# Performance work log

Measured on AMD Instinct MI355X. Metric: run time of the kernel, lower is better.

The kernel has to match this reference:

```python
import jax, jax.numpy as jnp
import numpy as np

EMBED = 1024
HEADS = 16
HEAD_DIM = EMBED // HEADS


def setup_inputs() -> dict:
    key = jax.random.key(0)
    ks = jax.random.split(key, 8)
    N, S = 4, 2048
    values = jax.random.normal(ks[0], (N, S, EMBED), dtype=jnp.float32)
    queries = jax.random.normal(ks[1], (N, S, EMBED), dtype=jnp.float32)
    keys = jax.random.normal(ks[2], (N, S, EMBED), dtype=jnp.float32)
    mask = jax.random.randint(ks[3], (N, 1, S, S), 0, 2, dtype=jnp.int32)
    sc = 1.0 / np.sqrt(HEAD_DIM)
    Wv = jax.random.normal(ks[4], (HEAD_DIM, HEAD_DIM), dtype=jnp.float32) * sc
    Wk = jax.random.normal(ks[5], (HEAD_DIM, HEAD_DIM), dtype=jnp.float32) * sc
    Wq = jax.random.normal(ks[6], (HEAD_DIM, HEAD_DIM), dtype=jnp.float32) * sc
    Wo = jax.random.normal(ks[7], (EMBED, EMBED), dtype=jnp.float32) * (1.0 / np.sqrt(EMBED))
    bo = jnp.zeros((EMBED,), dtype=jnp.float32)
    return {"values": values, "queries": queries, "keys": keys, "mask": mask,
            "Wv": Wv, "Wk": Wk, "Wq": Wq, "Wo": Wo, "bo": bo}


def reference(values, queries, keys, mask, Wv, Wk, Wq, Wo, bo):
    N, S, _ = queries.shape
    # split heads: (N, len, H, D)
    v = values.reshape(N, -1, HEADS, HEAD_DIM)
    k = keys.reshape(N, -1, HEADS, HEAD_DIM)
    q = queries.reshape(N, -1, HEADS, HEAD_DIM)
    # per-head linear projections (nn.Linear: y = x @ W.T, no bias)
    v = jnp.einsum('nlhd,ed->nlhe', v, Wv)
    k = jnp.einsum('nlhd,ed->nlhe', k, Wk)
    q = jnp.einsum('nlhd,ed->nlhe', q, Wq)
    # energy: (N, H, q_len, k_len)
    energy = jnp.einsum('nqhd,nkhd->nhqk', q, k)
    energy = jnp.where(mask == 0, jnp.float32(-1e20), energy)
    # non-standard scale: sqrt(embed_size), applied after masking
    attn = jax.nn.softmax(energy / jnp.sqrt(jnp.float32(EMBED)), axis=3)
    out = jnp.einsum('nhql,nlhd->nqhd', attn, v).reshape(N, S, EMBED)
    return out @ Wo.T + bo
```

## Files before the change

### kernel.cpp

```cpp
#include <hip/hip_runtime.h>
#include <hip/hip_bf16.h>

#define NBATCH 4
#define SEQ    2048
#define EMBED  1024
#define HEADS  16
#define HD     64

typedef __attribute__((ext_vector_type(8))) short bf16x8;
typedef __attribute__((ext_vector_type(4))) float f32x4;

__device__ __forceinline__ short f2bf(float f) {
  union { float f; unsigned u; } v; v.f = f;
  unsigned r = v.u + 0x7fffu + ((v.u >> 16) & 1u);
  return (short)(r >> 16);
}

__device__ __forceinline__ unsigned pkbf(float a, float b) {
#if __has_builtin(__builtin_amdgcn_cvt_pk_bf16_f32)
  typedef __attribute__((ext_vector_type(2))) __bf16 bf16x2_t;
  bf16x2_t r = __builtin_amdgcn_cvt_pk_bf16_f32(a, b);
  union { bf16x2_t v; unsigned u; } cv; cv.v = r; return cv.u;
#else
  return (unsigned)(unsigned short)f2bf(a) | ((unsigned)(unsigned short)f2bf(b) << 16);
#endif
}

typedef __attribute__((address_space(1))) const void gas_void;
typedef __attribute__((address_space(3))) void las_void;
__device__ __forceinline__ void glds16(const void* g, void* l) {
  __builtin_amdgcn_global_load_lds((gas_void*)g, (las_void*)l, 16, 0, 0);
}

#define C2 0.04508422f

__global__ __launch_bounds__(256) void cvt_all(
    const float* __restrict__ Wo, const float* __restrict__ Wq,
    const float* __restrict__ Wk, const float* __restrict__ Wv,
    short* __restrict__ dWo, short* __restrict__ dWq,
    short* __restrict__ dWk, short* __restrict__ dWv)
{
  int e = (blockIdx.x * 256 + threadIdx.x) * 4;
  const float* src; short* dst; int off; float sc = 1.0f;
  if (e < EMBED * EMBED) { src = Wo; dst = dWo; off = e; }
  else {
    int j = e - EMBED * EMBED;
    if      (j < 4096)  { src = Wq; dst = dWq; off = j; sc = C2; }
    else if (j < 8192)  { src = Wk; dst = dWk; off = j - 4096; }
    else if (j < 12288) { src = Wv; dst = dWv; off = j - 8192; }
    else return;
  }
  float4 v = *(const float4*)(src + off);
  ushort4 p;
  p.x = (unsigned short)f2bf(v.x * sc);
  p.y = (unsigned short)f2bf(v.y * sc);
  p.z = (unsigned short)f2bf(v.z * sc);
  p.w = (unsigned short)f2bf(v.w * sc);
  *(ushort4*)(dst + off) = p;
}

__global__ __launch_bounds__(256) void mask_pack(const int* __restrict__ mask,
                                                 unsigned long long* __restrict__ bits) {
  long long t = (long long)blockIdx.x * 256 + threadIdx.x;
  int lane = threadIdx.x & 63;
  int m = mask[t];
  unsigned long long b = __ballot(m != 0);
  if (lane == 0) bits[t >> 6] = b;
}

__global__ __launch_bounds__(256) void proj_kernel(
    const float* __restrict__ srcQ, const float* __restrict__ srcK, const float* __restrict__ srcV,
    const short* __restrict__ WbQ, const short* __restrict__ WbK, const short* __restrict__ WbV,
    short* __restrict__ Qp, short* __restrict__ Kp, short* __restrict__ Vt)
{
  int rt = blockIdx.x;
  int h  = blockIdx.y;
  int mz = blockIdx.z;
  const float* src = (mz == 0) ? srcQ : ((mz == 1) ? srcK : srcV);
  const short* Wb  = (mz == 0) ? WbQ : ((mz == 1) ? WbK : WbV);

  __shared__ __align__(16) short At[64][72];

  int tid = threadIdx.x;
  int r0 = rt * 64;
  for (int idx = tid; idx < 64 * 16; idx += 256) {
    int row = idx >> 4;
    int c4  = idx & 15;
    float4 v = *(const float4*)(src + (long long)(r0 + row) * EMBED + h * HD + c4 * 4);
    uint2 pk2;
    pk2.x = pkbf(v.x, v.y);
    pk2.y = pkbf(v.z, v.w);
    *(uint2*)&At[row][c4 * 4] = pk2;
  }
  __syncthreads();

  int lane = tid & 63, w = tid >> 6, quad = lane >> 4, l15 = lane & 15;

  bf16x8 af0 = *(const bf16x8*)&At[w * 16 + l15][quad * 8];
  bf16x8 af1 = *(const bf16x8*)&At[w * 16 + l15][32 + quad * 8];

  f32x4 acc[4];
  for (int cg = 0; cg < 4; cg++) {
    acc[cg] = (f32x4){0.f, 0.f, 0.f, 0.f};
    bf16x8 b0 = *(const bf16x8*)(Wb + (cg * 16 + l15) * 64 + quad * 8);
    bf16x8 b1 = *(const bf16x8*)(Wb + (cg * 16 + l15) * 64 + 32 + quad * 8);
    acc[cg] = __builtin_amdgcn_mfma_f32_16x16x32_bf16(af0, b0, acc[cg], 0, 0, 0);
    acc[cg] = __builtin_amdgcn_mfma_f32_16x16x32_bf16(af1, b1, acc[cg], 0, 0, 0);
  }

  int rloc = w * 16 + quad * 4;
  if (mz < 2) {
    short* dst = (mz == 0) ? Qp : Kp;
    for (int cg = 0; cg < 4; cg++) {
      for (int reg = 0; reg < 4; reg++) {
        int r = r0 + rloc + reg;
        int n = r >> 11, s = r & 2047;
        dst[((long long)(n * HEADS + h) * SEQ + s) * HD + cg * 16 + l15] = f2bf(acc[cg][reg]);
      }
    }
  } else {
    int r = r0 + rloc;
    int n = r >> 11, s = r & 2047;
    for (int cg = 0; cg < 4; cg++) {
      int d = cg * 16 + l15;
      uint2 pk2;
      pk2.x = pkbf(acc[cg][0], acc[cg][1]);
      pk2.y = pkbf(acc[cg][2], acc[cg][3]);
      *(uint2*)(Vt + ((long long)(n * HEADS + h) * HD + d) * SEQ + s) = pk2;
    }
  }
}

__global__ __launch_bounds__(512) void attn_kernel(
    const short* __restrict__ Qp, const short* __restrict__ Kp, const short* __restrict__ Vt,
    const unsigned long long* __restrict__ mbits, short* __restrict__ AO)
{
  int qt = blockIdx.x, h = blockIdx.y, nb = blockIdx.z;
  int q0 = qt * 128;

  __shared__ __align__(16) short KtL[2][64 * 64];
  __shared__ __align__(16) short VsL[2][64 * 64];
  __shared__ __align__(16) short Pls[8][16][72];

  int tid = threadIdx.x, lane = tid & 63, w = tid >> 6, quad = lane >> 4, l15 = lane & 15;
  int g8 = lane & 7, r8 = lane >> 3;
  int swz = g8 ^ r8;
  int s3 = l15 & 7;
  int o0 = (quad ^ s3) * 16;
  int o1 = ((quad + 4) ^ s3) * 16;

  long long nh = (long long)(nb * HEADS + h);
  const char* Kb = (const char*)(Kp + nh * SEQ * HD);
  const char* Vb = (const char*)(Vt + nh * HD * SEQ);
  const short* Qbase = Qp + (nh * SEQ + q0) * HD;

  int qrow = q0 + w * 16 + l15;

  int kgo = (w * 8 + r8) * 128 + swz * 16;
  int vgo = (w * 8 + r8) * 4096 + swz * 16;
  unsigned klo = (unsigned)(w * 8) * 128;

  const unsigned long long* mptr = mbits + ((long long)nb * SEQ + qrow) * 32;

  bf16x8 qf0 = *(const bf16x8*)(Qbase + (w * 16 + l15) * HD + quad * 8);
  bf16x8 qf1 = *(const bf16x8*)(Qbase + (w * 16 + l15) * HD + 32 + quad * 8);

  f32x4 O[4];
#pragma unroll
  for (int i = 0; i < 4; i++) O[i] = (f32x4){0.f, 0.f, 0.f, 0.f};
  float lsum = 0.f;

  glds16(Kb + kgo, (char*)KtL[0] + klo);
  glds16(Vb + vgo, (char*)VsL[0] + klo);
  unsigned long long mrow_nxt = mptr[0];

  for (int kt = 0; kt < 32; kt++) {
    __syncthreads();

    if (kt < 31) {
      int k1 = (kt + 1) * 64;
      glds16(Kb + k1 * 128 + kgo, (char*)KtL[(kt + 1) & 1] + klo);
      glds16(Vb + k1 * 2   + vgo, (char*)VsL[(kt + 1) & 1] + klo);
    }
    unsigned long long mrow = mrow_nxt;
    if (kt < 31) mrow_nxt = mptr[kt + 1];

    const char* KB = (const char*)KtL[kt & 1];
    f32x4 sA[4];
#pragma unroll
    for (int cg = 0; cg < 4; cg++) {
      bf16x8 kf0 = *(const bf16x8*)(KB + (cg * 16 + l15) * 128 + o0);
      bf16x8 kf1 = *(const bf16x8*)(KB + (cg * 16 + l15) * 128 + o1);
      f32x4 a = (f32x4){0.f, 0.f, 0.f, 0.f};
      a = __builtin_amdgcn_mfma_f32_16x16x32_bf16(kf0, qf0, a, 0, 0, 0);
      a = __builtin_amdgcn_mfma_f32_16x16x32_bf16(kf1, qf1, a, 0, 0, 0);
      sA[cg] = a;
    }

    unsigned mlo = (unsigned)mrow, mhi = (unsigned)(mrow >> 32);
    unsigned sh = (unsigned)(quad * 4);
    unsigned nibs[4];
    nibs[0] = (mlo >> sh) & 0xFu;
    nibs[1] = (mlo >> (sh + 16)) & 0xFu;
    nibs[2] = (mhi >> sh) & 0xFu;
    nibs[3] = (mhi >> (sh + 16)) & 0xFu;

#pragma unroll
    for (int cg = 0; cg < 4; cg++) {
#pragma unroll
      for (int r = 0; r < 4; r++) {
        float p = __builtin_amdgcn_exp2f(sA[cg][r]);
        p = (nibs[cg] & (1u << r)) ? p : 0.f;
        sA[cg][r] = p;
      }
    }
    {
      float a0 = (sA[0][0] + sA[0][1]) + (sA[0][2] + sA[0][3]);
      float a1 = (sA[1][0] + sA[1][1]) + (sA[1][2] + sA[1][3]);
      float a2 = (sA[2][0] + sA[2][1]) + (sA[2][2] + sA[2][3]);
      float a3 = (sA[3][0] + sA[3][1]) + (sA[3][2] + sA[3][3]);
      lsum += (a0 + a1) + (a2 + a3);
    }

#pragma unroll
    for (int cg = 0; cg < 4; cg++) {
      uint2 pk;
      pk.x = pkbf(sA[cg][0], sA[cg][1]);
      pk.y = pkbf(sA[cg][2], sA[cg][3]);
      *(uint2*)&Pls[w][l15][cg * 16 + quad * 4] = pk;
    }

    bf16x8 pa0 = *(const bf16x8*)&Pls[w][l15][quad * 8];
    bf16x8 pa1 = *(const bf16x8*)&Pls[w][l15][32 + quad * 8];

    const char* VB = (const char*)VsL[kt & 1];
#pragma unroll
    for (int cg = 0; cg < 4; cg++) {
      bf16x8 vf0 = *(const bf16x8*)(VB + (cg * 16 + l15) * 128 + o0);
      bf16x8 vf1 = *(const bf16x8*)(VB + (cg * 16 + l15) * 128 + o1);
      O[cg] = __builtin_amdgcn_mfma_f32_16x16x32_bf16(vf0, pa0, O[cg], 0, 0, 0);
      O[cg] = __builtin_amdgcn_mfma_f32_16x16x32_bf16(vf1, pa1, O[cg], 0, 0, 0);
    }
  }

  lsum += __shfl_xor(lsum, 16);
  lsum += __shfl_xor(lsum, 32);
  float inv = 1.f / lsum;
  short* aoRow = AO + ((long long)nb * SEQ + qrow) * EMBED + h * HD;
#pragma unroll
  for (int cg = 0; cg < 4; cg++) {
    uint2 pk;
    pk.x = pkbf(O[cg][0] * inv, O[cg][1] * inv);
    pk.y = pkbf(O[cg][2] * inv, O[cg][3] * inv);
    *(uint2*)(aoRow + cg * 16 + quad * 4) = pk;
  }
}

__global__ __launch_bounds__(256) void outproj_kernel(
    const short* __restrict__ AO, const short* __restrict__ Wob,
    const float* __restrict__ bo, float* __restrict__ out)
{
  int rt = blockIdx.x, ct = blockIdx.y;
  __shared__ __align__(16) short AtL[128 * 64];
  __shared__ __align__(16) short BtL[128 * 64];

  int tid = threadIdx.x, lane = tid & 63, w = tid >> 6, quad = lane >> 4, l15 = lane & 15;
  int g8 = lane & 7, r8 = lane >> 3;
  int swz = g8 ^ r8;
  int s3 = l15 & 7;
  int o0 = (quad ^ s3) * 16;
  int o1 = ((quad + 4) ^ s3) * 16;

  int r0 = rt * 128, c0 = ct * 128;
  int wr = (w >> 1) * 64, wc = (w & 1) * 64;

  const char* Abase = (const char*)AO  + (long long)(r0 + w * 8 + r8) * 2048 + swz * 16;
  const char* Bbase = (const char*)Wob + (long long)(c0 + w * 8 + r8) * 2048 + swz * 16;
  unsigned lbase = (unsigned)(w * 8) * 128;

  f32x4 acc[4][4];
#pragma unroll
  for (int mi = 0; mi < 4; mi++)
#pragma unroll
    for (int ni = 0; ni < 4; ni++) acc[mi][ni] = (f32x4){0.f, 0.f, 0.f, 0.f};

  for (int kc = 0; kc < 16; kc++) {
    __syncthreads();
#pragma unroll
    for (int i = 0; i < 4; i++) {
      glds16(Abase + (long long)i * 32 * 2048 + kc * 128, (char*)AtL + lbase + i * 32 * 128);
      glds16(Bbase + (long long)i * 32 * 2048 + kc * 128, (char*)BtL + lbase + i * 32 * 128);
    }
    __syncthreads();

    const char* AB = (const char*)AtL;
    const char* BB = (const char*)BtL;
    bf16x8 af[4][2], bf[4][2];
#pragma unroll
    for (int mi = 0; mi < 4; mi++) {
      int r = wr + mi * 16 + l15;
      af[mi][0] = *(const bf16x8*)(AB + r * 128 + o0);
      af[mi][1] = *(const bf16x8*)(AB + r * 128 + o1);
    }
#pragma unroll
    for (int ni = 0; ni < 4; ni++) {
      int r = wc + ni * 16 + l15;
      bf[ni][0] = *(const bf16x8*)(BB + r * 128 + o0);
      bf[ni][1] = *(const bf16x8*)(BB + r * 128 + o1);
    }
#pragma unroll
    for (int mi = 0; mi < 4; mi++)
#pragma unroll
      for (int ni = 0; ni < 4; ni++) {
        acc[mi][ni] = __builtin_amdgcn_mfma_f32_16x16x32_bf16(af[mi][0], bf[ni][0], acc[mi][ni], 0, 0, 0);
        acc[mi][ni] = __builtin_amdgcn_mfma_f32_16x16x32_bf16(af[mi][1], bf[ni][1], acc[mi][ni], 0, 0, 0);
      }
  }

#pragma unroll
  for (int ni = 0; ni < 4; ni++) {
    float b = bo[c0 + wc + ni * 16 + l15];
#pragma unroll
    for (int mi = 0; mi < 4; mi++)
#pragma unroll
      for (int reg = 0; reg < 4; reg++) {
        int r = r0 + wr + mi * 16 + quad * 4 + reg;
        out[(long long)r * EMBED + c0 + wc + ni * 16 + l15] = acc[mi][ni][reg] + b;
      }
  }
}

extern "C" void kernel_launch(void* const* d_in, const int* in_sizes, int n_in,
                              void* d_out, int out_size, void* d_ws, size_t ws_size,
                              hipStream_t stream) {
  const float* values  = (const float*)d_in[0];
  const float* queries = (const float*)d_in[1];
  const float* keys    = (const float*)d_in[2];
  const int*   mask    = (const int*)d_in[3];
  const float* Wv = (const float*)d_in[4];
  const float* Wk = (const float*)d_in[5];
  const float* Wq = (const float*)d_in[6];
  const float* Wo = (const float*)d_in[7];
  const float* bo = (const float*)d_in[8];
  float* out = (float*)d_out;

  char* ws = (char*)d_ws;
  size_t off = 0;
  const size_t PROJ_BYTES = (size_t)NBATCH * HEADS * SEQ * HD * 2;
  short* Qp = (short*)(ws + off); off += PROJ_BYTES;
  short* Kp = (short*)(ws + off); off += PROJ_BYTES;
  short* Vt = (short*)(ws + off); off += PROJ_BYTES;
  short* AO = (short*)(ws + off); off += PROJ_BYTES;
  unsigned long long* mbits = (unsigned long long*)(ws + off);
  off += (size_t)NBATCH * SEQ * (SEQ / 64) * 8;
  short* Wob = (short*)(ws + off); off += (size_t)EMBED * EMBED * 2;
  short* WbQ = (short*)(ws + off); off += HD * HD * 2;
  short* WbK = (short*)(ws + off); off += HD * HD * 2;
  short* WbV = (short*)(ws + off); off += HD * HD * 2;

  cvt_all<<<dim3((EMBED * EMBED + 3 * HD * HD) / 4 / 256), dim3(256), 0, stream>>>(
      Wo, Wq, Wk, Wv, Wob, WbQ, WbK, WbV);

  mask_pack<<<dim3((NBATCH * SEQ * SEQ) / 256), dim3(256), 0, stream>>>(mask, mbits);

  proj_kernel<<<dim3((NBATCH * SEQ) / 64, HEADS, 3), dim3(256), 0, stream>>>(
      queries, keys, values, WbQ, WbK, WbV, Qp, Kp, Vt);

  attn_kernel<<<dim3(SEQ / 128, HEADS, NBATCH), dim3(512), 0, stream>>>(Qp, Kp, Vt, mbits, AO);

  outproj_kernel<<<dim3((NBATCH * SEQ) / 128, EMBED / 128), dim3(256), 0, stream>>>(AO, Wob, bo, out);
}
```

Baseline: 377.1 us.

## Rewrite attention with 32x32 MFMA, in-register P via permlane32 swap

The attention kernel now uses 32x32x16 bf16 MFMA tiles with 4 waves each owning 32 query rows, instead of 16x16x32 tiles with 8 waves. The softmax probabilities are repacked in registers with v_permlane32_swap into the B-operand layout, removing the per-wave LDS round trip for P. The loop is manually unrolled by two so buffer indices are compile-time constants. This aims to cut LDS traffic and instruction overhead and raise MFMA efficiency, at the cost of more registers per thread and fewer threads per block.

```diff
diff --git a/kernel.cpp b/kernel.cpp
--- a/kernel.cpp
+++ b/kernel.cpp
@@ -9,6 +9,7 @@
 
 typedef __attribute__((ext_vector_type(8))) short bf16x8;
 typedef __attribute__((ext_vector_type(4))) float f32x4;
+typedef __attribute__((ext_vector_type(16))) float f32x16;
 
 __device__ __forceinline__ short f2bf(float f) {
   union { float f; unsigned u; } v; v.f = f;
@@ -31,6 +32,17 @@
 __device__ __forceinline__ void glds16(const void* g, void* l) {
   __builtin_amdgcn_global_load_lds((gas_void*)g, (las_void*)l, 16, 0, 0);
 }
+
+__device__ __forceinline__ bf16x8 mk8(unsigned a, unsigned b, unsigned c, unsigned d) {
+  union { unsigned u[4]; bf16x8 v; } t;
+  t.u[0] = a; t.u[1] = b; t.u[2] = c; t.u[3] = d; return t.v;
+}
+
+__device__ __forceinline__ void pl32swap(unsigned &a, unsigned &b) {
+  asm volatile("v_permlane32_swap_b32 %0, %1" : "+v"(a), "+v"(b));
+}
+
+#define MFMA32(A, B, C) __builtin_amdgcn_mfma_f32_32x32x16_bf16((A), (B), (C), 0, 0, 0)
 
 #define C2 0.04508422f
 
@@ -131,128 +143,148 @@
   }
 }
 
-__global__ __launch_bounds__(512) void attn_kernel(
+#define SOFTMAX_KK(SV, MW, PAV0, PAV1) do {                                       \
+    unsigned n0 = ((MW) >> sh4) & 0xFu;                                           \
+    unsigned n1 = ((MW) >> (sh4 + 8)) & 0xFu;                                     \
+    unsigned n2 = ((MW) >> (sh4 + 16)) & 0xFu;                                    \
+    unsigned n3 = ((MW) >> (sh4 + 24)) & 0xFu;                                    \
+    float p0  = __builtin_amdgcn_exp2f(SV[0]);   p0  = (n0 & 1u) ? p0  : 0.f;     \
+    float p1  = __builtin_amdgcn_exp2f(SV[1]);   p1  = (n0 & 2u) ? p1  : 0.f;     \
+    float p2  = __builtin_amdgcn_exp2f(SV[2]);   p2  = (n0 & 4u) ? p2  : 0.f;     \
+    float p3  = __builtin_amdgcn_exp2f(SV[3]);   p3  = (n0 & 8u) ? p3  : 0.f;     \
+    float p4  = __builtin_amdgcn_exp2f(SV[4]);   p4  = (n1 & 1u) ? p4  : 0.f;     \
+    float p5  = __builtin_amdgcn_exp2f(SV[5]);   p5  = (n1 & 2u) ? p5  : 0.f;     \
+    float p6  = __builtin_amdgcn_exp2f(SV[6]);   p6  = (n1 & 4u) ? p6  : 0.f;     \
+    float p7  = __builtin_amdgcn_exp2f(SV[7]);   p7  = (n1 & 8u) ? p7  : 0.f;     \
+    float p8  = __builtin_amdgcn_exp2f(SV[8]);   p8  = (n2 & 1u) ? p8  : 0.f;     \
+    float p9  = __builtin_amdgcn_exp2f(SV[9]);   p9  = (n2 & 2u) ? p9  : 0.f;     \
+    float p10 = __builtin_amdgcn_exp2f(SV[10]);  p10 = (n2 & 4u) ? p10 : 0.f;     \
+    float p11 = __builtin_amdgcn_exp2f(SV[11]);  p11 = (n2 & 8u) ? p11 : 0.f;     \
+    float p12 = __builtin_amdgcn_exp2f(SV[12]);  p12 = (n3 & 1u) ? p12 : 0.f;     \
+    float p13 = __builtin_amdgcn_exp2f(SV[13]);  p13 = (n3 & 2u) ? p13 : 0.f;     \
+    float p14 = __builtin_amdgcn_exp2f(SV[14]);  p14 = (n3 & 4u) ? p14 : 0.f;     \
+    float p15 = __builtin_amdgcn_exp2f(SV[15]);  p15 = (n3 & 8u) ? p15 : 0.f;     \
+    lsum += (((p0 + p1) + (p2 + p3)) + ((p4 + p5) + (p6 + p7)))                   \
+          + (((p8 + p9) + (p10 + p11)) + ((p12 + p13) + (p14 + p15)));            \
+    unsigned u0 = pkbf(p0, p1),   u1 = pkbf(p2, p3);                              \
+    unsigned u2 = pkbf(p4, p5),   u3 = pkbf(p6, p7);                              \
+    unsigned u4 = pkbf(p8, p9),   u5 = pkbf(p10, p11);                            \
+    unsigned u6 = pkbf(p12, p13), u7 = pkbf(p14, p15);                            \
+    pl32swap(u0, u2); pl32swap(u1, u3);                                           \
+    pl32swap(u4, u6); pl32swap(u5, u7);                                           \
+    PAV0 = mk8(u0, u1, u2, u3);                                                   \
+    PAV1 = mk8(u4, u5, u6, u7);                                                   \
+  } while (0)
+
+#define ATTN_ITER(BUF, KT) do {                                                   \
+    __syncthreads();                                                              \
+    if ((KT) < 31) {                                                              \
+      const char* ks_ = Kb + ((KT) + 1) * 8192 + kgo;                             \
+      const char* vs_ = Vb + ((KT) + 1) * 128 + vgo;                              \
+      char* kd_ = ldsK + (((BUF) ^ 1) * 8192) + klo;                              \
+      char* vd_ = ldsV + (((BUF) ^ 1) * 8192) + klo;                              \
+      glds16(ks_,          kd_);                                                  \
+      glds16(ks_ + 4096,   kd_ + 4096);                                           \
+      glds16(vs_,          vd_);                                                  \
+      glds16(vs_ + 131072, vd_ + 4096);                                           \
+      mnxt = mptr[(KT) + 1];                                                      \
+    }                                                                             \
+    unsigned mlo = (unsigned)mcur, mhiw = (unsigned)(mcur >> 32);                 \
+    const char* KB_ = ldsK + (BUF) * 8192;                                        \
+    const char* VB_ = ldsV + (BUF) * 8192;                                        \
+    bf16x8 pa0, pa1, pa2, pa3;                                                    \
+    {                                                                             \
+      f32x16 s = {};                                                              \
+      s = MFMA32(*(const bf16x8*)(KB_ + a4_0), qf0, s);                           \
+      s = MFMA32(*(const bf16x8*)(KB_ + a4_1), qf1, s);                           \
+      s = MFMA32(*(const bf16x8*)(KB_ + a4_2), qf2, s);                           \
+      s = MFMA32(*(const bf16x8*)(KB_ + a4_3), qf3, s);                           \
+      SOFTMAX_KK(s, mlo, pa0, pa1);                                               \
+    }                                                                             \
+    {                                                                             \
+      f32x16 s = {};                                                              \
+      s = MFMA32(*(const bf16x8*)(KB_ + 4096 + a4_0), qf0, s);                    \
+      s = MFMA32(*(const bf16x8*)(KB_ + 4096 + a4_1), qf1, s);                    \
+      s = MFMA32(*(const bf16x8*)(KB_ + 4096 + a4_2), qf2, s);                    \
+      s = MFMA32(*(const bf16x8*)(KB_ + 4096 + a4_3), qf3, s);                    \
+      SOFTMAX_KK(s, mhiw, pa2, pa3);                                              \
+    }                                                                             \
+    O0 = MFMA32(*(const bf16x8*)(VB_ + a4_0),        pa0, O0);                    \
+    O1 = MFMA32(*(const bf16x8*)(VB_ + 4096 + a4_0), pa0, O1);                    \
+    O0 = MFMA32(*(const bf16x8*)(VB_ + a4_1),        pa1, O0);                    \
+    O1 = MFMA32(*(const bf16x8*)(VB_ + 4096 + a4_1), pa1, O1);                    \
+    O0 = MFMA32(*(const bf16x8*)(VB_ + a4_2),        pa2, O0);                    \
+    O1 = MFMA32(*(const bf16x8*)(VB_ + 4096 + a4_2), pa2, O1);                    \
+    O0 = MFMA32(*(const bf16x8*)(VB_ + a4_3),        pa3, O0);                    \
+    O1 = MFMA32(*(const bf16x8*)(VB_ + 4096 + a4_3), pa3, O1);                    \
+    mcur = mnxt;                                                                  \
+  } while (0)
+
+__global__ __launch_bounds__(256, 4) void attn_kernel(
     const short* __restrict__ Qp, const short* __restrict__ Kp, const short* __restrict__ Vt,
     const unsigned long long* __restrict__ mbits, short* __restrict__ AO)
 {
   int qt = blockIdx.x, h = blockIdx.y, nb = blockIdx.z;
   int q0 = qt * 128;
 
-  __shared__ __align__(16) short KtL[2][64 * 64];
-  __shared__ __align__(16) short VsL[2][64 * 64];
-  __shared__ __align__(16) short Pls[8][16][72];
-
-  int tid = threadIdx.x, lane = tid & 63, w = tid >> 6, quad = lane >> 4, l15 = lane & 15;
+  __shared__ __align__(16) char ldsK[2 * 8192];
+  __shared__ __align__(16) char ldsV[2 * 8192];
+
+  int tid = threadIdx.x, lane = tid & 63, w = tid >> 6;
+  int l31 = lane & 31, hi5 = lane >> 5;
   int g8 = lane & 7, r8 = lane >> 3;
-  int swz = g8 ^ r8;
-  int s3 = l15 & 7;
-  int o0 = (quad ^ s3) * 16;
-  int o1 = ((quad + 4) ^ s3) * 16;
+  int pp = lane & 7;
+  unsigned sh4 = (unsigned)(hi5 * 4);
 
   long long nh = (long long)(nb * HEADS + h);
   const char* Kb = (const char*)(Kp + nh * SEQ * HD);
   const char* Vb = (const char*)(Vt + nh * HD * SEQ);
-  const short* Qbase = Qp + (nh * SEQ + q0) * HD;
-
-  int qrow = q0 + w * 16 + l15;
-
-  int kgo = (w * 8 + r8) * 128 + swz * 16;
-  int vgo = (w * 8 + r8) * 4096 + swz * 16;
-  unsigned klo = (unsigned)(w * 8) * 128;
+
+  int kgo = (w * 8 + r8) * 128 + ((g8 ^ r8) << 4);
+  int vgo = (w * 8 + r8) * 4096 + ((g8 ^ r8) << 4);
+  int klo = w * 1024;
+
+  int a4_0 = l31 * 128 + ((((0 | hi5) ^ pp)) << 4);
+  int a4_1 = l31 * 128 + ((((2 | hi5) ^ pp)) << 4);
+  int a4_2 = l31 * 128 + ((((4 | hi5) ^ pp)) << 4);
+  int a4_3 = l31 * 128 + ((((6 | hi5) ^ pp)) << 4);
+
+  int qrow = q0 + w * 32 + l31;
+  const short* Qb = Qp + (nh * SEQ + qrow) * HD + hi5 * 8;
+  bf16x8 qf0 = *(const bf16x8*)(Qb);
+  bf16x8 qf1 = *(const bf16x8*)(Qb + 16);
+  bf16x8 qf2 = *(const bf16x8*)(Qb + 32);
+  bf16x8 qf3 = *(const bf16x8*)(Qb + 48);
 
   const unsigned long long* mptr = mbits + ((long long)nb * SEQ + qrow) * 32;
 
-  bf16x8 qf0 = *(const bf16x8*)(Qbase + (w * 16 + l15) * HD + quad * 8);
-  bf16x8 qf1 = *(const bf16x8*)(Qbase + (w * 16 + l15) * HD + 32 + quad * 8);
-
-  f32x4 O[4];
-#pragma unroll
-  for (int i = 0; i < 4; i++) O[i] = (f32x4){0.f, 0.f, 0.f, 0.f};
+  f32x16 O0 = {}, O1 = {};
   float lsum = 0.f;
 
-  glds16(Kb + kgo, (char*)KtL[0] + klo);
-  glds16(Vb + vgo, (char*)VsL[0] + klo);
-  unsigned long long mrow_nxt = mptr[0];
-
-  for (int kt = 0; kt < 32; kt++) {
-    __syncthreads();
-
-    if (kt < 31) {
-      int k1 = (kt + 1) * 64;
-      glds16(Kb + k1 * 128 + kgo, (char*)KtL[(kt + 1) & 1] + klo);
-      glds16(Vb + k1 * 2   + vgo, (char*)VsL[(kt + 1) & 1] + klo);
-    }
-    unsigned long long mrow = mrow_nxt;
-    if (kt < 31) mrow_nxt = mptr[kt + 1];
-
-    const char* KB = (const char*)KtL[kt & 1];
-    f32x4 sA[4];
-#pragma unroll
-    for (int cg = 0; cg < 4; cg++) {
-      bf16x8 kf0 = *(const bf16x8*)(KB + (cg * 16 + l15) * 128 + o0);
-      bf16x8 kf1 = *(const bf16x8*)(KB + (cg * 16 + l15) * 128 + o1);
-      f32x4 a = (f32x4){0.f, 0.f, 0.f, 0.f};
-      a = __builtin_amdgcn_mfma_f32_16x16x32_bf16(kf0, qf0, a, 0, 0, 0);
-      a = __builtin_amdgcn_mfma_f32_16x16x32_bf16(kf1, qf1, a, 0, 0, 0);
-      sA[cg] = a;
-    }
-
-    unsigned mlo = (unsigned)mrow, mhi = (unsigned)(mrow >> 32);
-    unsigned sh = (unsigned)(quad * 4);
-    unsigned nibs[4];
-    nibs[0] = (mlo >> sh) & 0xFu;
-    nibs[1] = (mlo >> (sh + 16)) & 0xFu;
-    nibs[2] = (mhi >> sh) & 0xFu;
-    nibs[3] = (mhi >> (sh + 16)) & 0xFu;
-
-#pragma unroll
-    for (int cg = 0; cg < 4; cg++) {
-#pragma unroll
-      for (int r = 0; r < 4; r++) {
-        float p = __builtin_amdgcn_exp2f(sA[cg][r]);
-        p = (nibs[cg] & (1u << r)) ? p : 0.f;
-        sA[cg][r] = p;
-      }
-    }
-    {
-      float a0 = (sA[0][0] + sA[0][1]) + (sA[0][2] + sA[0][3]);
-      float a1 = (sA[1][0] + sA[1][1]) + (sA[1][2] + sA[1][3]);
-      float a2 = (sA[2][0] + sA[2][1]) + (sA[2][2] + sA[2][3]);
-      float a3 = (sA[3][0] + sA[3][1]) + (sA[3][2] + sA[3][3]);
-      lsum += (a0 + a1) + (a2 + a3);
-    }
-
-#pragma unroll
-    for (int cg = 0; cg < 4; cg++) {
-      uint2 pk;
-      pk.x = pkbf(sA[cg][0], sA[cg][1]);
-      pk.y = pkbf(sA[cg][2], sA[cg][3]);
-      *(uint2*)&Pls[w][l15][cg * 16 + quad * 4] = pk;
-    }
-
-    bf16x8 pa0 = *(const bf16x8*)&Pls[w][l15][quad * 8];
-    bf16x8 pa1 = *(const bf16x8*)&Pls[w][l15][32 + quad * 8];
-
-    const char* VB = (const char*)VsL[kt & 1];
-#pragma unroll
-    for (int cg = 0; cg < 4; cg++) {
-      bf16x8 vf0 = *(const bf16x8*)(VB + (cg * 16 + l15) * 128 + o0);
-      bf16x8 vf1 = *(const bf16x8*)(VB + (cg * 16 + l15) * 128 + o1);
-      O[cg] = __builtin_amdgcn_mfma_f32_16x16x32_bf16(vf0, pa0, O[cg], 0, 0, 0);
-      O[cg] = __builtin_amdgcn_mfma_f32_16x16x32_bf16(vf1, pa1, O[cg], 0, 0, 0);
-    }
-  }
-
-  lsum += __shfl_xor(lsum, 16);
+  glds16(Kb + kgo,          ldsK + klo);
+  glds16(Kb + 4096 + kgo,   ldsK + 4096 + klo);
+  glds16(Vb + vgo,          ldsV + klo);
+  glds16(Vb + vgo + 131072, ldsV + 4096 + klo);
+  unsigned long long mcur = mptr[0], mnxt = 0;
+
+  for (int it = 0; it < 16; it++) {
+    ATTN_ITER(0, it * 2);
+    ATTN_ITER(1, it * 2 + 1);
+  }
+
   lsum += __shfl_xor(lsum, 32);
   float inv = 1.f / lsum;
-  short* aoRow = AO + ((long long)nb * SEQ + qrow) * EMBED + h * HD;
-#pragma unroll
-  for (int cg = 0; cg < 4; cg++) {
+
+  short* aoRow = AO + ((long long)nb * SEQ + qrow) * EMBED + h * HD + hi5 * 4;
+#pragma unroll
+  for (int j = 0; j < 4; j++) {
     uint2 pk;
-    pk.x = pkbf(O[cg][0] * inv, O[cg][1] * inv);
-    pk.y = pkbf(O[cg][2] * inv, O[cg][3] * inv);
-    *(uint2*)(aoRow + cg * 16 + quad * 4) = pk;
+    pk.x = pkbf(O0[4 * j] * inv, O0[4 * j + 1] * inv);
+    pk.y = pkbf(O0[4 * j + 2] * inv, O0[4 * j + 3] * inv);
+    *(uint2*)(aoRow + j * 8) = pk;
+    pk.x = pkbf(O1[4 * j] * inv, O1[4 * j + 1] * inv);
+    pk.y = pkbf(O1[4 * j + 2] * inv, O1[4 * j + 3] * inv);
+    *(uint2*)(aoRow + 32 + j * 8) = pk;
   }
 }
 
@@ -366,7 +398,7 @@
   proj_kernel<<<dim3((NBATCH * SEQ) / 64, HEADS, 3), dim3(256), 0, stream>>>(
       queries, keys, values, WbQ, WbK, WbV, Qp, Kp, Vt);
 
-  attn_kernel<<<dim3(SEQ / 128, HEADS, NBATCH), dim3(512), 0, stream>>>(Qp, Kp, Vt, mbits, AO);
+  attn_kernel<<<dim3(SEQ / 128, HEADS, NBATCH), dim3(256), 0, stream>>>(Qp, Kp, Vt, mbits, AO);
 
   outproj_kernel<<<dim3((NBATCH * SEQ) / 128, EMBED / 128), dim3(256), 0, stream>>>(AO, Wob, bo, out);
 }
```

After: 386.8 us. 1.03x slower.
